# Kernel tuning notes

Measured on AMD Instinct MI355X. Metric: run time of the kernel, lower is better.

## Reference

```python
import jax, jax.numpy as jnp
import numpy as np

B, IN_F, OUT_F = 1024, 256, 256
GRID_SIZE, K = 5, 3  # grid_size, spline_order
N_BASIS = GRID_SIZE + K


def _make_grid():
    h = (1.0 - (-1.0)) / GRID_SIZE
    return jnp.linspace(-1.0 - K * h, 1.0 + K * h, GRID_SIZE + 2 * K + 1, dtype=jnp.float32)


def compute_bspline_basis(x, grid, k):
    # x: (N,), grid: (G + 2k + 1,) -> (N, G + k)
    x = x[:, None]
    bases = ((x >= grid[:-1]) & (x < grid[1:])).astype(x.dtype)
    for p in range(1, k + 1):
        n = bases.shape[1] - 1
        left_den = jnp.clip(grid[p:p + n] - grid[:n], 1e-8)
        left = (x - grid[:n]) / left_den * bases[:, :n]
        right_den = jnp.clip(grid[p + 1:p + 1 + n] - grid[1:1 + n], 1e-8)
        right = (grid[p + 1:p + 1 + n] - x) / right_den * bases[:, 1:1 + n]
        bases = left + right
    # boundary fix: x at/above last interior knot falls into last basis
    bases = bases.at[:, -1].add((x[:, 0] >= grid[-k - 1]).astype(x.dtype))
    return bases


def setup_inputs() -> dict:
    key = jax.random.key(0)
    kx, kc, kb = jax.random.split(key, 3)
    x = jax.random.normal(kx, (B, IN_F), dtype=jnp.float32)
    coeff = jax.random.normal(kc, (OUT_F, IN_F, N_BASIS), dtype=jnp.float32) / np.sqrt(IN_F * N_BASIS)
    base_weight = jax.random.normal(kb, (OUT_F, IN_F), dtype=jnp.float32) / np.sqrt(IN_F)
    spline_weight = jnp.ones((OUT_F, IN_F), dtype=jnp.float32)
    grid = _make_grid()
    return {"x": x, "grid": grid, "coeff": coeff,
            "base_weight": base_weight, "spline_weight": spline_weight}


def reference(x, grid, coeff, base_weight, spline_weight):
    batch = x.shape[0]
    bases = compute_bspline_basis(x.reshape(-1), grid, K)          # (B*in, n_basis)
    bases = bases.reshape(batch, IN_F, N_BASIS)                     # (b, i, n)
    spline_out = jnp.einsum('bin,oin->boi', bases, coeff)           # (b, o, i)
    spline_out = spline_out * spline_weight[None, :, :]
    base_out = jax.nn.silu(x)[:, None, :] * base_weight[None, :, :]  # (b, o, i)
    return (spline_out + base_out).sum(axis=2)                      # (b, o)
```

## Files before the change

### kernel.cpp

```cpp
#include <hip/hip_runtime.h>
#include <hip/hip_bf16.h>

#define B_SZ   1024
#define IN_F   256
#define OUT_F  256
#define NB     9
#define KTOT   (IN_F * NB)
#define NGRID  12

typedef __attribute__((ext_vector_type(8))) short bf16x8;
typedef __attribute__((ext_vector_type(4))) float f32x4;

__global__ __launch_bounds__(256) void kan_features(
    const float* __restrict__ x,
    const float* __restrict__ grid,
    __hip_bfloat16* __restrict__ phi) {
  int idx = blockIdx.x * 256 + threadIdx.x;

  float g[NGRID];
#pragma unroll
  for (int j = 0; j < NGRID; ++j) g[j] = grid[j];

  float xv = x[idx];

  float bas[NGRID - 1];
#pragma unroll
  for (int j = 0; j < NGRID - 1; ++j)
    bas[j] = (xv >= g[j] && xv < g[j + 1]) ? 1.0f : 0.0f;

#pragma unroll
  for (int p = 1; p <= 3; ++p) {
    int n = NGRID - 1 - p;
#pragma unroll
    for (int j = 0; j < n; ++j) {
      float ld = g[p + j] - g[j];
      if (ld < 1e-8f) ld = 1e-8f;
      float rd = g[p + 1 + j] - g[j + 1];
      if (rd < 1e-8f) rd = 1e-8f;
      bas[j] = (xv - g[j]) * __builtin_amdgcn_rcpf(ld) * bas[j] +
               (g[p + 1 + j] - xv) * __builtin_amdgcn_rcpf(rd) * bas[j + 1];
    }
  }
  bas[7] += (xv >= g[NGRID - 4]) ? 1.0f : 0.0f;

  float sil = xv / (1.0f + __expf(-xv));

  int b = idx >> 8;
  int i = idx & 255;
  __hip_bfloat16* dst = phi + b * KTOT + i;
#pragma unroll
  for (int n = 0; n < 8; ++n) dst[n * IN_F] = __float2bfloat16(bas[n]);
  dst[8 * IN_F] = __float2bfloat16(sil);
}

__global__ __launch_bounds__(256) void kan_weights(
    const float* __restrict__ coeff,
    const float* __restrict__ bw,
    const float* __restrict__ sw,
    __hip_bfloat16* __restrict__ W) {
  int idx = blockIdx.x * 256 + threadIdx.x;
  int o = idx >> 8;
  int i = idx & 255;
  float s = sw[idx];
  const float* c = coeff + (size_t)idx * 8;
  __hip_bfloat16* dst = W + o * KTOT + i;
#pragma unroll
  for (int n = 0; n < 8; ++n)
    dst[n * IN_F] = __float2bfloat16(s * c[n]);
  dst[8 * IN_F] = __float2bfloat16(bw[idx]);
}

__global__ __launch_bounds__(256) void kan_gemm(
    const __hip_bfloat16* __restrict__ phi,
    const __hip_bfloat16* __restrict__ W,
    float* __restrict__ out) {
  int wave = ((blockIdx.x * 256) + threadIdx.x) >> 6;
  int lane = threadIdx.x & 63;
  int to = wave & 15;
  int tb = wave >> 4;
  int m = lane & 15;
  int q = lane >> 4;

  const short* ap = (const short*)(phi + (tb * 16 + m) * KTOT + q * 8);
  const short* bp = (const short*)(W + (to * 16 + m) * KTOT + q * 8);

  f32x4 acc = {0.f, 0.f, 0.f, 0.f};
#pragma unroll 8
  for (int k = 0; k < KTOT; k += 32) {
    bf16x8 a = *(const bf16x8*)(ap + k);
    bf16x8 b = *(const bf16x8*)(bp + k);
    acc = __builtin_amdgcn_mfma_f32_16x16x32_bf16(a, b, acc, 0, 0, 0);
  }

  int row = tb * 16 + q * 4;
  int col = to * 16 + m;
#pragma unroll
  for (int r = 0; r < 4; ++r)
    out[(row + r) * OUT_F + col] = acc[r];
}

extern "C" void kernel_launch(void* const* d_in, const int* in_sizes, int n_in,
                              void* d_out, int out_size, void* d_ws, size_t ws_size,
                              hipStream_t stream) {
  const float* x     = (const float*)d_in[0];
  const float* grid  = (const float*)d_in[1];
  const float* coeff = (const float*)d_in[2];
  const float* bw    = (const float*)d_in[3];
  const float* sw    = (const float*)d_in[4];
  float* out = (float*)d_out;

  __hip_bfloat16* phi = (__hip_bfloat16*)d_ws;
  __hip_bfloat16* W   = phi + (size_t)B_SZ * KTOT;

  kan_features<<<(B_SZ * IN_F) / 256, 256, 0, stream>>>(x, grid, phi);
  kan_weights<<<(OUT_F * IN_F) / 256, 256, 0, stream>>>(coeff, bw, sw, W);
  kan_gemm<<<(B_SZ / 16) * (OUT_F / 16) / 4, 256, 0, stream>>>(phi, W, out);
}
```

Baseline: 87.65 us.

## Merge prep kernels and use split-K 32x32 MFMA GEMM with LDS reduction

The feature and weight preparation kernels are merged into a single launch, with the block index selecting which work a block does. The GEMM moves from one 16x16 output tile per wave to 32x32 tiles per 512-thread block. The eight waves split the K dimension and use 32x32x16 bf16 MFMA, then their partial sums are reduced through shared memory. This is meant to cut a launch, give each wave more output per load and more parallelism along K, at the cost of 32KB of LDS and a barrier per block.

Result: faster. 76.75 us (-12.4%).

```diff
diff --git a/kernel.cpp b/kernel.cpp
--- a/kernel.cpp
+++ b/kernel.cpp
@@ -8,95 +8,113 @@
 #define KTOT   (IN_F * NB)
 #define NGRID  12
 
-typedef __attribute__((ext_vector_type(8))) short bf16x8;
-typedef __attribute__((ext_vector_type(4))) float f32x4;
+typedef __attribute__((ext_vector_type(8))) short  bf16x8;
+typedef __attribute__((ext_vector_type(16))) float f32x16;
 
-__global__ __launch_bounds__(256) void kan_features(
+__global__ __launch_bounds__(256) void kan_prep(
     const float* __restrict__ x,
     const float* __restrict__ grid,
-    __hip_bfloat16* __restrict__ phi) {
-  int idx = blockIdx.x * 256 + threadIdx.x;
-
-  float g[NGRID];
-#pragma unroll
-  for (int j = 0; j < NGRID; ++j) g[j] = grid[j];
-
-  float xv = x[idx];
-
-  float bas[NGRID - 1];
-#pragma unroll
-  for (int j = 0; j < NGRID - 1; ++j)
-    bas[j] = (xv >= g[j] && xv < g[j + 1]) ? 1.0f : 0.0f;
-
-#pragma unroll
-  for (int p = 1; p <= 3; ++p) {
-    int n = NGRID - 1 - p;
-#pragma unroll
-    for (int j = 0; j < n; ++j) {
-      float ld = g[p + j] - g[j];
-      if (ld < 1e-8f) ld = 1e-8f;
-      float rd = g[p + 1 + j] - g[j + 1];
-      if (rd < 1e-8f) rd = 1e-8f;
-      bas[j] = (xv - g[j]) * __builtin_amdgcn_rcpf(ld) * bas[j] +
-               (g[p + 1 + j] - xv) * __builtin_amdgcn_rcpf(rd) * bas[j + 1];
-    }
-  }
-  bas[7] += (xv >= g[NGRID - 4]) ? 1.0f : 0.0f;
-
-  float sil = xv / (1.0f + __expf(-xv));
-
-  int b = idx >> 8;
-  int i = idx & 255;
-  __hip_bfloat16* dst = phi + b * KTOT + i;
-#pragma unroll
-  for (int n = 0; n < 8; ++n) dst[n * IN_F] = __float2bfloat16(bas[n]);
-  dst[8 * IN_F] = __float2bfloat16(sil);
-}
-
-__global__ __launch_bounds__(256) void kan_weights(
     const float* __restrict__ coeff,
     const float* __restrict__ bw,
     const float* __restrict__ sw,
+    __hip_bfloat16* __restrict__ phi,
     __hip_bfloat16* __restrict__ W) {
-  int idx = blockIdx.x * 256 + threadIdx.x;
-  int o = idx >> 8;
-  int i = idx & 255;
-  float s = sw[idx];
-  const float* c = coeff + (size_t)idx * 8;
-  __hip_bfloat16* dst = W + o * KTOT + i;
+  if (blockIdx.x < (B_SZ * IN_F) / 256) {
+    int idx = blockIdx.x * 256 + threadIdx.x;
+    float g[NGRID];
 #pragma unroll
-  for (int n = 0; n < 8; ++n)
-    dst[n * IN_F] = __float2bfloat16(s * c[n]);
-  dst[8 * IN_F] = __float2bfloat16(bw[idx]);
+    for (int j = 0; j < NGRID; ++j) g[j] = grid[j];
+    float xv = x[idx];
+
+    float bas[NGRID - 1];
+#pragma unroll
+    for (int j = 0; j < NGRID - 1; ++j)
+      bas[j] = (xv >= g[j] && xv < g[j + 1]) ? 1.0f : 0.0f;
+
+#pragma unroll
+    for (int p = 1; p <= 3; ++p) {
+      int n = NGRID - 1 - p;
+#pragma unroll
+      for (int j = 0; j < n; ++j) {
+        float ld = g[p + j] - g[j];
+        if (ld < 1e-8f) ld = 1e-8f;
+        float rd = g[p + 1 + j] - g[j + 1];
+        if (rd < 1e-8f) rd = 1e-8f;
+        bas[j] = (xv - g[j]) * __builtin_amdgcn_rcpf(ld) * bas[j] +
+                 (g[p + 1 + j] - xv) * __builtin_amdgcn_rcpf(rd) * bas[j + 1];
+      }
+    }
+    bas[7] += (xv >= g[NGRID - 4]) ? 1.0f : 0.0f;
+    float sil = xv / (1.0f + __expf(-xv));
+
+    int b = idx >> 8;
+    int i = idx & 255;
+    __hip_bfloat16* dst = phi + b * KTOT + i;
+#pragma unroll
+    for (int n = 0; n < 8; ++n) dst[n * IN_F] = __float2bfloat16(bas[n]);
+    dst[8 * IN_F] = __float2bfloat16(sil);
+  } else {
+    int idx = (blockIdx.x - (B_SZ * IN_F) / 256) * 256 + threadIdx.x;
+    int o = idx >> 8;
+    int i = idx & 255;
+    float s = sw[idx];
+    const float* c = coeff + (size_t)idx * 8;
+    __hip_bfloat16* dst = W + o * KTOT + i;
+#pragma unroll
+    for (int n = 0; n < 8; ++n)
+      dst[n * IN_F] = __float2bfloat16(s * c[n]);
+    dst[8 * IN_F] = __float2bfloat16(bw[idx]);
+  }
 }
 
-__global__ __launch_bounds__(256) void kan_gemm(
+#define KSEG (KTOT / 8)
+
+__global__ __launch_bounds__(512) void kan_gemm(
     const __hip_bfloat16* __restrict__ phi,
     const __hip_bfloat16* __restrict__ W,
     float* __restrict__ out) {
-  int wave = ((blockIdx.x * 256) + threadIdx.x) >> 6;
-  int lane = threadIdx.x & 63;
-  int to = wave & 15;
-  int tb = wave >> 4;
-  int m = lane & 15;
-  int q = lane >> 4;
+  __shared__ float partial[8][32 * 32];
 
-  const short* ap = (const short*)(phi + (tb * 16 + m) * KTOT + q * 8);
-  const short* bp = (const short*)(W + (to * 16 + m) * KTOT + q * 8);
+  int tid  = threadIdx.x;
+  int wave = tid >> 6;
+  int lane = tid & 63;
+  int bm = (blockIdx.x & 31) * 32;
+  int bn = (blockIdx.x >> 5) * 32;
+  int r = lane & 31;
+  int h = lane >> 5;
 
-  f32x4 acc = {0.f, 0.f, 0.f, 0.f};
-#pragma unroll 8
-  for (int k = 0; k < KTOT; k += 32) {
+  const short* ap = (const short*)(phi + (size_t)(bm + r) * KTOT) + wave * KSEG + h * 8;
+  const short* bp = (const short*)(W   + (size_t)(bn + r) * KTOT) + wave * KSEG + h * 8;
+
+  f32x16 acc;
+#pragma unroll
+  for (int g = 0; g < 16; ++g) acc[g] = 0.0f;
+
+#pragma unroll 6
+  for (int k = 0; k < KSEG; k += 16) {
     bf16x8 a = *(const bf16x8*)(ap + k);
     bf16x8 b = *(const bf16x8*)(bp + k);
-    acc = __builtin_amdgcn_mfma_f32_16x16x32_bf16(a, b, acc, 0, 0, 0);
+    acc = __builtin_amdgcn_mfma_f32_32x32x16_bf16(a, b, acc, 0, 0, 0);
   }
 
-  int row = tb * 16 + q * 4;
-  int col = to * 16 + m;
+  float* pw = &partial[wave][0];
 #pragma unroll
-  for (int r = 0; r < 4; ++r)
-    out[(row + r) * OUT_F + col] = acc[r];
+  for (int g = 0; g < 16; ++g) {
+    int row = (g & 3) + 8 * (g >> 2) + 4 * h;
+    pw[row * 32 + r] = acc[g];
+  }
+  __syncthreads();
+
+  int e0 = tid * 2;
+  float s0 = 0.0f, s1 = 0.0f;
+#pragma unroll
+  for (int w = 0; w < 8; ++w) {
+    s0 += partial[w][e0];
+    s1 += partial[w][e0 + 1];
+  }
+  int row = e0 >> 5, col = e0 & 31;
+  float2 v = make_float2(s0, s1);
+  *(float2*)&out[(size_t)(bm + row) * OUT_F + bn + col] = v;
 }
 
 extern "C" void kernel_launch(void* const* d_in, const int* in_sizes, int n_in,
@@ -112,7 +130,7 @@
   __hip_bfloat16* phi = (__hip_bfloat16*)d_ws;
   __hip_bfloat16* W   = phi + (size_t)B_SZ * KTOT;
 
-  kan_features<<<(B_SZ * IN_F) / 256, 256, 0, stream>>>(x, grid, phi);
-  kan_weights<<<(OUT_F * IN_F) / 256, 256, 0, stream>>>(coeff, bw, sw, W);
-  kan_gemm<<<(B_SZ / 16) * (OUT_F / 16) / 4, 256, 0, stream>>>(phi, W, out);
+  kan_prep<<<(B_SZ * IN_F + OUT_F * IN_F) / 256, 256, 0, stream>>>(
+      x, grid, coeff, bw, sw, phi, W);
+  kan_gemm<<<(B_SZ / 32) * (OUT_F / 32), 512, 0, stream>>>(phi, W, out);
 }
```
